# Optimization experiments

Measured on AMD Instinct MI355X. Metric: run time of the kernel, lower is better.

Reference implementation:

```python
import jax, jax.numpy as jnp
import numpy as np

D = 1024          # feature dim (x_dim)
C = 32            # n classes (way)
SHOTS = 32
N_SUP = C * SHOTS
Q = 1024
REG = 0.5         # reg_param


def setup_inputs() -> dict:
    key = jax.random.key(0)
    ks = jax.random.split(key, 5)
    support_x = jax.random.normal(ks[0], (N_SUP, D), dtype=jnp.float32)
    query_x = jax.random.normal(ks[1], (Q, D), dtype=jnp.float32)
    labels_idx = (jnp.arange(N_SUP, dtype=jnp.int32) % C)  # every class present, equal shots
    m = jax.random.normal(ks[2], (1, D), dtype=jnp.float32) * 0.01
    kappa = jnp.float32(0.1)
    nu = jnp.float32(D)
    triu_diag = jnp.ones((D,), dtype=jnp.float32)
    triu_lower = jnp.eye(D, dtype=jnp.float32) + 0.01 * jax.random.normal(ks[3], (D, D), dtype=jnp.float32)
    return {"support_x": support_x, "query_x": query_x, "labels_idx": labels_idx,
            "m": m, "kappa": kappa, "nu": nu,
            "triu_diag": triu_diag, "triu_lower": triu_lower}


def _metaqda_fb(support_x, query_x, labels_idx, m, kappa, nu, triu_diag, triu_lower):
    onehot = jax.nn.one_hot(labels_idx, C, dtype=support_x.dtype)      # [N, C]
    Nj = jnp.sum(onehot, axis=0)                                       # [C]
    kappa_ = jnp.abs(kappa) + 1e-6
    nu_ = jnp.maximum(nu, jnp.float32(D - 1 + 1e-6))

    # Cholesky-factor prior scatter matrix: L @ L^T
    lower_mask = jnp.tril(jnp.ones((D, D), dtype=support_x.dtype), k=-1)
    L = jnp.diag(jnp.abs(triu_diag)) + triu_lower * lower_mask
    prior_S = L @ L.T                                                  # [D, D]

    # per-class sums (replaces python loop of rank-1 outer products with GEMMs)
    sum_x = onehot.T @ support_x                                       # [C, D]
    mean_x = sum_x / Nj[:, None]
    # sum_n x x^T per class: contract through [N,C,D] intermediate
    SXX = jnp.einsum('nc,nd,ne->cde', onehot, support_x, support_x)    # [C, D, D]

    kN = kappa_ + Nj                                                   # [C]
    mu = (kappa_ / kN)[:, None] * m + (Nj / kN)[:, None] * mean_x      # [C, D]

    mm = m.T @ m                                                       # [D, D]  (self_outer of [1,D])
    mumu = jnp.einsum('cd,ce->cde', mu, mu)                            # [C, D, D]
    S = prior_S[None] + SXX + kappa_ * mm[None] - kN[:, None, None] * mumu

    scale = (kN + 1.0) / ((nu_ + Nj - D + 1.0) * kN)                   # [C]
    sigma = S * scale[:, None, None]                                   # [C, D, D]

    sigma_inv = (1.0 - REG) * jnp.linalg.inv(sigma) + REG * jnp.eye(D, dtype=sigma.dtype)

    common = nu_ + Nj + 1.0 - D                                        # [C]
    _, logdet = jnp.linalg.slogdet(sigma)
    bias = (jax.lax.lgamma(0.5 * (common + D)) - jax.lax.lgamma(0.5 * common)
            - 0.5 * D * jnp.log(common) - 0.5 * logdet)                # [C]

    diff = query_x[:, None, :] - mu[None, :, :]                        # [Q, C, D]
    dist = jnp.einsum('qcd,cde,qce->qc', diff, sigma_inv, diff)        # [Q, C]
    preds = bias[None, :] - 0.5 * (common + D)[None, :] * jnp.log1p(dist / common[None, :])
    return preds


def reference(support_x, query_x, labels_idx, m, kappa, nu, triu_diag, triu_lower):
    return _metaqda_fb(support_x, query_x, labels_idx, m, kappa, nu, triu_diag, triu_lower)
```

## Files before the change

### kernel.cpp

```cpp
#include <hip/hip_runtime.h>
#include <math.h>

#define Dk 1024
#define Ck 32
#define Nk 1024
#define Qk 1024
#define REGP 0.5f
#define NB 64
#define NROWSV (Qk + Nk + Ck + 1)

#define CO_KAPPA 0
#define CO_NU    1
#define CO_NJ    2
#define CO_KN    34
#define CO_SCALE 66
#define CO_COMMON 98
#define CO_COEF  130
#define CO_BIASA 162
#define CO_BIASF 200

#define O_P    0u
#define O_W    2162688u
#define O_T    3211264u
#define O_MU   3473408u
#define O_QM   3506176u
#define O_MB   3538944u
#define O_MI   3578112u
#define O_QNY  3617280u
#define O_QNO  3618304u
#define O_MUN  3619328u
#define O_GMM  3619360u
#define O_EX   3619392u
#define O_CONS 3619408u
#define O_CIDX 3619664u
#define O_YH   3652432u
#define O_YM   4733776u
#define O_YL   5815120u
#define O_WH   6896464u
#define O_WM   7420752u
#define O_WL   7945040u
#define O_OH   8469328u
#define O_OM   9550672u
#define O_OL   10632016u

#define WS_DECL \
    float* P     = Wbuf + O_P;    (void)P; \
    float* W     = Wbuf + O_W;    (void)W; \
    float* Tb    = Wbuf + O_T;    (void)Tb; \
    float* QM    = Wbuf + O_QM;   (void)QM; \
    float* Mbuf  = Wbuf + O_MB;   (void)Mbuf; \
    float* Minv  = Wbuf + O_MI;   (void)Minv; \
    float* qny   = Wbuf + O_QNY;  (void)qny; \
    float* qno   = Wbuf + O_QNO;  (void)qno; \
    float* mun2o = Wbuf + O_MUN;  (void)mun2o; \
    float* gmm   = Wbuf + O_GMM;  (void)gmm; \
    float* extraf= Wbuf + O_EX;   (void)extraf; \
    float* cons  = Wbuf + O_CONS; (void)cons; \
    int*   cidx  = (int*)(Wbuf + O_CIDX); (void)cidx; \
    ushort* sYh = (ushort*)(Wbuf + O_YH); (void)sYh; \
    ushort* sYm = (ushort*)(Wbuf + O_YM); (void)sYm; \
    ushort* sYl = (ushort*)(Wbuf + O_YL); (void)sYl; \
    ushort* sWh = (ushort*)(Wbuf + O_WH); (void)sWh; \
    ushort* sWm = (ushort*)(Wbuf + O_WM); (void)sWm; \
    ushort* sWl = (ushort*)(Wbuf + O_WL); (void)sWl; \
    ushort* sOh = (ushort*)(Wbuf + O_OH); (void)sOh; \
    ushort* sOm = (ushort*)(Wbuf + O_OM); (void)sOm; \
    ushort* sOl = (ushort*)(Wbuf + O_OL); (void)sOl;

typedef __attribute__((ext_vector_type(8))) __bf16 bf16x8;
typedef __attribute__((ext_vector_type(4))) float f32x4;

#define MFMA(a, b, c) __builtin_amdgcn_mfma_f32_16x16x32_bf16(a, b, c, 0, 0, 0)

__device__ __forceinline__ ushort f2bf(float x) {
    unsigned u = __float_as_uint(x);
    return (ushort)((u + 0x7FFFu + ((u >> 16) & 1u)) >> 16);
}
__device__ __forceinline__ float bf2f(ushort h) {
    return __uint_as_float(((unsigned)h) << 16);
}
__device__ __forceinline__ void split1(float x, ushort& h, ushort& m, ushort& l) {
    h = f2bf(x);
    float r1 = x - bf2f(h);
    m = f2bf(r1);
    l = f2bf(r1 - bf2f(m));
}
__device__ __forceinline__ void split_store4(ushort* ph, ushort* pm, ushort* pl,
                                             size_t o, float4 v) {
    float vv[4] = {v.x, v.y, v.z, v.w};
    ushort4 H, M, L;
    ushort* Hp = (ushort*)&H; ushort* Mp = (ushort*)&M; ushort* Lp = (ushort*)&L;
#pragma unroll
    for (int c = 0; c < 4; ++c) split1(vv[c], Hp[c], Mp[c], Lp[c]);
    *(ushort4*)(ph + o) = H;
    *(ushort4*)(pm + o) = M;
    *(ushort4*)(pl + o) = L;
}

__device__ __forceinline__ float wave_red(float s) {
#pragma unroll
    for (int o = 32; o > 0; o >>= 1) s += __shfl_down(s, o, 64);
    return s;
}

#define LDSB3(c, r, k8) ((c) * 5120 + (r) * 40 + (k8))
#define LDS_HW3 15360

__device__ __forceinline__ void b_fetch3(bf16x8* rb,
                                         const ushort* Bh, const ushort* Bm, const ushort* Bl,
                                         int bRow0, int kcol, int t) {
#pragma unroll
    for (int u = 0; u < 6; ++u) {
        int comp = u >> 1;
        int idx = ((u & 1) << 8) + t;
        int row = idx >> 2, kg = idx & 3;
        const ushort* Bs = (comp == 0) ? Bh : ((comp == 1) ? Bm : Bl);
        rb[u] = *(const bf16x8*)(Bs + (size_t)(bRow0 + row) * 1024 + kcol + kg * 8);
    }
}
__device__ __forceinline__ void b_store3(ushort* lds, const bf16x8* rb, int t) {
#pragma unroll
    for (int u = 0; u < 6; ++u) {
        int comp = u >> 1;
        int idx = ((u & 1) << 8) + t;
        int row = idx >> 2, kg = idx & 3;
        *(bf16x8*)(lds + LDSB3(comp, row, kg * 8)) = rb[u];
    }
}
__device__ __forceinline__ void a_fetch3(bf16x8 af[4][3],
                                         const ushort* Ah, const ushort* Am, const ushort* Al,
                                         int arowT, int aRowMax, int kcol, int lk) {
    bf16x8 z = {};
#pragma unroll
    for (int rf = 0; rf < 4; ++rf) {
        int gr = arowT + rf * 16;
        bool ok = gr < aRowMax;
#pragma unroll
        for (int c = 0; c < 3; ++c) {
            const ushort* As = (c == 0) ? Ah : ((c == 1) ? Am : Al);
            af[rf][c] = ok ? *(const bf16x8*)(As + (size_t)gr * 1024 + kcol + lk * 8) : z;
        }
    }
}

__device__ __forceinline__ void tile_compute3(const ushort* lds, f32x4 acc[4][4],
                                              bf16x8 af[4][3], int bcol0, int lr, int lk) {
#pragma unroll
    for (int cf = 0; cf < 4; ++cf) {
        int brow = bcol0 + cf * 16 + lr;
        bf16x8 bh = *(const bf16x8*)(lds + LDSB3(0, brow, lk * 8));
        bf16x8 bm = *(const bf16x8*)(lds + LDSB3(1, brow, lk * 8));
        bf16x8 bl = *(const bf16x8*)(lds + LDSB3(2, brow, lk * 8));
#pragma unroll
        for (int rf = 0; rf < 4; ++rf) {
            f32x4 a = acc[rf][cf];
            a = MFMA(af[rf][0], bh, a);
            a = MFMA(af[rf][0], bm, a);
            a = MFMA(af[rf][1], bh, a);
            a = MFMA(af[rf][0], bl, a);
            a = MFMA(af[rf][2], bh, a);
            a = MFMA(af[rf][1], bm, a);
            acc[rf][cf] = a;
        }
    }
}

__device__ __forceinline__ void tile_gemm3(
    ushort* lds, f32x4 acc[4][4],
    const ushort* Ah, const ushort* Am, const ushort* Al, int aRow0, int aRowMax,
    const ushort* Bh, const ushort* Bm, const ushort* Bl, int bRow0,
    int kbase, int ksteps, int t)
{
    const int w = t >> 6, lr = t & 15, lk = (t >> 4) & 3;
    const int arowT = aRow0 + (w >> 1) * 64 + lr;
    const int bcol0 = (w & 1) * 64;
    bf16x8 rb[6], afc[4][3], afn[4][3];
    b_fetch3(rb, Bh, Bm, Bl, bRow0, kbase * 32, t);
    a_fetch3(afc, Ah, Am, Al, arowT, aRowMax, kbase * 32, lk);
    b_store3(lds, rb, t);
    __syncthreads();
    for (int kt = 0; kt < ksteps; ++kt) {
        if (kt + 1 < ksteps) {
            b_fetch3(rb, Bh, Bm, Bl, bRow0, (kbase + kt + 1) * 32, t);
            a_fetch3(afn, Ah, Am, Al, arowT, aRowMax, (kbase + kt + 1) * 32, lk);
        }
        tile_compute3(lds, acc, afc, bcol0, lr, lk);
        __syncthreads();
        if (kt + 1 < ksteps) {
            b_store3(lds, rb, t);
#pragma unroll
            for (int rf = 0; rf < 4; ++rf)
#pragma unroll
                for (int c = 0; c < 3; ++c) afc[rf][c] = afn[rf][c];
        }
        __syncthreads();
    }
}

__device__ __forceinline__ void fetch4(float4* reg, const float* src, int ld,
                                       int rowbase, int rowmax, int colbase, int t) {
#pragma unroll
    for (int u = 0; u < 4; ++u) {
        int slot = t + u * 256;
        int r = slot >> 4, c4 = slot & 15;
        int gr = rowbase + r;
        reg[u] = (gr < rowmax) ? *(const float4*)(src + (size_t)gr * ld + colbase + c4 * 4)
                               : make_float4(0.f, 0.f, 0.f, 0.f);
    }
}
__device__ __forceinline__ void stT(float* dst, const float4* reg, int t) {
#pragma unroll
    for (int u = 0; u < 4; ++u) {
        int slot = t + u * 256;
        int r = slot >> 4, c4 = slot & 15;
        dst[(c4 * 4 + 0) * 68 + r] = reg[u].x;
        dst[(c4 * 4 + 1) * 68 + r] = reg[u].y;
        dst[(c4 * 4 + 2) * 68 + r] = reg[u].z;
        dst[(c4 * 4 + 3) * 68 + r] = reg[u].w;
    }
}
__device__ __forceinline__ void stN(float* dst, const float4* reg, int t) {
#pragma unroll
    for (int u = 0; u < 4; ++u) {
        int slot = t + u * 256;
        int r = slot >> 4, c4 = slot & 15;
        *(float4*)(dst + r * 68 + c4 * 4) = reg[u];
    }
}
__device__ __forceinline__ void gemm16(const float* At, const float* Bt,
                                       float acc[4][4], int tx, int ty) {
#pragma unroll 4
    for (int kk = 0; kk < NB; ++kk) {
        float4 a = *(const float4*)(At + kk * 68 + ty * 4);
        float4 b = *(const float4*)(Bt + kk * 68 + tx * 4);
        float av[4] = {a.x, a.y, a.z, a.w};
        float bv[4] = {b.x, b.y, b.z, b.w};
#pragma unroll
        for (int r = 0; r < 4; ++r)
#pragma unroll
            for (int s = 0; s < 4; ++s) acc[r][s] += av[r] * bv[s];
    }
}
__device__ __forceinline__ void mm_task(
    const float* aSrc, int aLd, int aRow, int aRowMax, int aCol, int aRowStep, int aColStep,
    const float* bSrc, int bLd, int bRow, int bRowMax, int bCol, int bRowStep, int bColStep,
    bool bTrans, int k0, int k1,
    float acc[4][4], float* smA, float* smB, int t, int tx, int ty)
{
    float4 ra[4], rb[4];
    fetch4(ra, aSrc, aLd, aRow + k0 * aRowStep, aRowMax, aCol + k0 * aColStep, t);
    fetch4(rb, bSrc, bLd, bRow + k0 * bRowStep, bRowMax, bCol + k0 * bColStep, t);
    stT(smA, ra, t);
    if (bTrans) stT(smB, rb, t); else stN(smB, rb, t);
    __syncthreads();
    for (int kt = k0; kt < k1; ++kt) {
        if (kt + 1 < k1) {
            fetch4(ra, aSrc, aLd, aRow + (kt + 1) * aRowStep, aRowMax, aCol + (kt + 1) * aColStep, t);
            fetch4(rb, bSrc, bLd, bRow + (kt + 1) * bRowStep, bRowMax, bCol + (kt + 1) * bColStep, t);
        }
        gemm16(smA, smB, acc, tx, ty);
        __syncthreads();
        if (kt + 1 < k1) {
            stT(smA, ra, t);
            if (bTrans) stT(smB, rb, t); else stN(smB, rb, t);
        }
        __syncthreads();
    }
}

__global__ __launch_bounds__(256) void k_p0(const float* qx, const int* labels,
                                            const float* mvec, const float* kappa,
                                            const float* nu, const float* td,
                                            const float* tl, float* Wbuf) {
    __shared__ __align__(16) float smem[9216];
    float* sX  = smem + 8704;
    WS_DECL
    float* Yo32 = Wbuf;
    const int t = threadIdx.x;
    const int lane = t & 63, wv = t >> 6;
    const int tau = blockIdx.x;

    if (tau == 0) {
        int* scnt = (int*)sX;
        if (t < Ck) scnt[t] = 0;
        __syncthreads();
        for (int n = t; n < Nk; n += 256) {
            int l = labels[n];
            int pos = atomicAdd(&scnt[l], 1);
            cidx[l * Nk + pos] = n;
        }
        __syncthreads();
        if (t < Ck) {
            float kap = fabsf(kappa[0]) + 1e-6f;
            float nu_ = fmaxf(nu[0], (float)(Dk - 1) + 1e-6f);
            float Njf = (float)scnt[t];
            float kN = kap + Njf;
            if (t == 0) { cons[CO_KAPPA] = kap; cons[CO_NU] = nu_; }
            cons[CO_NJ + t] = Njf;
            cons[CO_KN + t] = kN;
            cons[CO_SCALE + t] = (kN + 1.0f) / ((nu_ + Njf - (float)Dk + 1.0f) * kN);
            float common = nu_ + Njf + 1.0f - (float)Dk;
            cons[CO_COMMON + t] = common;
            cons[CO_COEF + t] = 0.5f * (common + (float)Dk);
            cons[CO_BIASA + t] = lgammaf(0.5f * (common + (float)Dk)) - lgammaf(0.5f * common)
                                 - 0.5f * (float)Dk * logf(common);
        }
    } else if (tau == 1) {
        float s = 0.f;
        for (int i = t; i < Dk; i += 256) s += logf(fabsf(td[i]));
        s = wave_red(s);
        if (lane == 0) sX[wv] = s;
        __syncthreads();
        if (t == 0) extraf[0] = 2.f * (sX[0] + sX[1] + sX[2] + sX[3]);
    } else if (tau < 18) {
        int b0 = (tau - 2) * NB;
        for (int idx = t; idx < 64 * 64; idx += 256) {
            int m = idx >> 6, i = idx & 63;
            smem[i * 72 + m] = (m > i) ? tl[(size_t)(b0 + m) * Dk + b0 + i] : 0.f;
        }
        if (t < 64) smem[4608 + t] = 1.f / fabsf(td[b0 + t]);
        __syncthreads();
        if (t < 64) {
            const int j = t;
            float r[64];
#pragma unroll
            for (int m = 0; m < 64; ++m) r[m] = (m == j) ? 1.f : 0.f;
#pragma unroll
            for (int i = 0; i < 64; ++i) {
                float x = r[i] * smem[4608 + i];
                r[i] = x;
#pragma unroll
                for (int g = (i >> 2); g < 16; ++g) {
                    float4 lt = *(const float4*)&smem[i * 72 + g * 4];
                    r[g * 4 + 0] -= lt.x * x;
                    r[g * 4 + 1] -= lt.y * x;
                    r[g * 4 + 2] -= lt.z * x;
                    r[g * 4 + 3] -= lt.w * x;
                }
            }
#pragma unroll
            for (int i = 0; i < 64; ++i)
                W[(size_t)(b0 + i) * Dk + b0 + j] = r[i];
        }
    } else if (tau < 21) {
        int base = (tau - 18) * 13056;
        for (int i = t; i < 13056 && base + i < 39168; i += 256) Mbuf[base + i] = 0.f;
    } else if (tau == 21) {
        if (t < 32) { mun2o[t] = 0.f; gmm[t] = 0.f; }
        for (int i = t; i < 8192; i += 256)
            ((float4*)QM)[i] = make_float4(0, 0, 0, 0);
    } else if (tau < 86) {
        int rbase = (tau - 22) * 16;
        for (int j = wv; j < 16; j += 4) {
            const float* row = qx + (size_t)(rbase + j) * Dk;
            float s = 0.f;
            for (int d = lane; d < Dk; d += 64) { float v = row[d]; s += v * v; }
            s = wave_red(s);
            if (lane == 0) qno[rbase + j] = s;
        }
    } else if (tau < 150) {
        int rbase = (tau - 86) * 16;
        for (int j = 0; j < 16; ++j) {
            int r = rbase + j;
            float4 v = ((const float4*)(qx + (size_t)r * Dk))[t];
            split_store4(sYh, sYm, sYl, (size_t)r * 1024 + (size_t)t * 4, v);
        }
    } else if (tau == 150) {
        float4 v = ((const float4*)mvec)[t];
        split_store4(sYh, sYm, sYl, (size_t)2080 * 1024 + (size_t)t * 4, v);
    } else {
        int rbase = (tau - 151) * 16;
        for (int j = 0; j < 16; ++j)
            ((float4*)(Yo32 + (size_t)(rbase + j) * 1024))[t] = make_float4(0, 0, 0, 0);
    }
}

__global__ __launch_bounds__(256) void k_p1(const float* sx, const float* mvec,
                                            const float* tl, float* Wbuf) {
    __shared__ __align__(16) float smem[8704];
    WS_DECL
    const int t = threadIdx.x;
    const int lane = t & 63, wv = t >> 6;
    const int tau = blockIdx.x;
    if (tau < 128) {
        float* sX = smem;
        int c = tau >> 2;
        int d = ((tau & 3) << 8) + t;
        int Nj = (int)cons[CO_NJ + c];
        float kap = cons[CO_KAPPA], kN = cons[CO_KN + c];
        float acc = 0.f;
        for (int s = 0; s < Nj; ++s) acc += sx[(size_t)cidx[c * Nk + s] * Dk + d];
        float muv = (kap * mvec[d] + acc) / kN;
        size_t o = (size_t)(2048 + c) * 1024 + d;
        ushort h, m_, l_;
        split1(muv, h, m_, l_);
        sYh[o] = h; sYm[o] = m_; sYl[o] = l_;
        float s2 = wave_red(muv * muv);
        if (lane == 0) sX[wv] = s2;
        __syncthreads();
        if (t == 0) atomicAdd(&mun2o[c], sX[0] + sX[1] + sX[2] + sX[3]);
    } else if (tau < 192) {
        int rbase = (tau - 128) * 16;
        for (int j = 0; j < 16; ++j) {
            int n = rbase + j;
            int srcrow = cidx[(n >> 5) * Nk + (n & 31)];
            float4 v = ((const float4*)(sx + (size_t)srcrow * Dk))[t];
            split_store4(sYh, sYm, sYl, (size_t)(1024 + n) * 1024 + (size_t)t * 4, v);
        }
    } else {
        float* smA = smem;
        float* smB = smem + 4352;
        const int tx = t & 15, ty = t >> 4;
        const int BIG = 1 << 30;
        int pb = (tau - 192) * 128;
        float acc[4][4] = {};
        mm_task(tl, Dk, pb + 64, BIG, pb, 0, NB,
                W, Dk, pb, BIG, pb, NB, 0, false, 0, 1,
                acc, smA, smB, t, tx, ty);
        {
            float4 ra[4];
            fetch4(ra, W, Dk, pb + 64, BIG, pb + 64, t);
#pragma unroll
            for (int r = 0; r < 4; ++r)
#pragma unroll
                for (int s = 0; s < 4; ++s)
                    smB[(ty * 4 + r) * 68 + tx * 4 + s] = acc[r][s];
            stT(smA, ra, t);
        }
        __syncthreads();
        float acc2[4][4] = {};
        gemm16(smA, smB, acc2, tx, ty);
        __syncthreads();
#pragma unroll
        for (int r = 0; r < 4; ++r)
#pragma unroll
            for (int s = 0; s < 4; ++s)
                W[(size_t)(pb + 64 + ty * 4 + r) * Dk + pb + tx * 4 + s] = -acc2[r][s];
    }
}

__global__ __launch_bounds__(256) void k_tr_a(const float* tl, float* Wbuf, int h, int ht) {
    __shared__ __align__(16) float smem[8704];
    float* smA = smem;
    float* smB = smem + 4352;
    WS_DECL
    const int t = threadIdx.x;
    const int tx = t & 15, ty = t >> 4;
    const int BIG = 1 << 30;
    int tau = blockIdx.x;
    int p = tau / (ht * ht), rr = tau % (ht * ht);
    int i = rr / ht, j = rr % ht;
    int pb = p * 2 * h;
    float acc[4][4] = {};
    mm_task(tl, Dk, pb + h + i * NB, BIG, pb, 0, NB,
            W, Dk, pb, BIG, pb + j * NB, NB, 0, false, 0, ht,
            acc, smA, smB, t, tx, ty);
    float* Tp = Tb + (size_t)p * h * h;
#pragma unroll
    for (int r = 0; r < 4; ++r)
#pragma unroll
        for (int s = 0; s < 4; ++s)
            Tp[(size_t)(i * NB + ty * 4 + r) * h + j * NB + tx * 4 + s] = acc[r][s];
}

__global__ __launch_bounds__(256) void k_tr_b(float* Wbuf, int h, int ht) {
    __shared__ __align__(16) float smem[8704];
    float* smA = smem;
    float* smB = smem + 4352;
    WS_DECL
    const int t = threadIdx.x;
    const int tx = t & 15, ty = t >> 4;
    const int BIG = 1 << 30;
    int tau = blockIdx.x;
    int p = tau / (ht * ht), rr = tau % (ht * ht);
    int i = rr / ht, j = rr % ht;
    int pb = p * 2 * h;
    const float* Tp = Tb + (size_t)p * h * h;
    float acc[4][4] = {};
    mm_task(W, Dk, pb + h + i * NB, BIG, pb + h, 0, NB,
            Tp, h, 0, BIG, j * NB, NB, 0, false, 0, ht,
            acc, smA, smB, t, tx, ty);
#pragma unroll
    for (int r = 0; r < 4; ++r)
#pragma unroll
        for (int s = 0; s < 4; ++s)
            W[(size_t)(pb + h + i * NB + ty * 4 + r) * Dk + pb + j * NB + tx * 4 + s] = -acc[r][s];
}

__global__ __launch_bounds__(256) void k_cvtw(float* Wbuf) {
    WS_DECL
    const int t = threadIdx.x;
#pragma unroll
    for (int u = 0; u < 4; ++u) {
        unsigned g = blockIdx.x * 1024u + u * 256u + t;
        int row = g >> 8, col4 = (g & 255) * 4;
        float4 v = ((const float4*)W)[g];
        if (col4 + 0 > row) v.x = 0.f;
        if (col4 + 1 > row) v.y = 0.f;
        if (col4 + 2 > row) v.z = 0.f;
        if (col4 + 3 > row) v.w = 0.f;
        split_store4(sWh, sWm, sWl, (size_t)g * 4, v);
    }
}

__global__ __launch_bounds__(256) void k_yg(float* Wbuf) {
    __shared__ __align__(16) ushort lds[LDS_HW3];
    WS_DECL
    float* Yo32 = Wbuf;
    const int t = threadIdx.x;
    int b = blockIdx.x;
    int xcd = b & 7, pos = b >> 3;
    int e = (xcd < 4) ? xcd * 43 + pos : 172 + (xcd - 4) * 42 + pos;
    int q = e / 17, rt = e % 17;
    int jt2, kc;
    if (q < 4)       { jt2 = 7; kc = q; }
    else if (q < 8)  { jt2 = 6; kc = q - 4; }
    else if (q < 11) { jt2 = 5; kc = q - 8; }
    else if (q < 14) { jt2 = 4; kc = q - 11; }
    else if (q < 16) { jt2 = 3; kc = q - 14; }
    else if (q < 18) { jt2 = 2; kc = q - 16; }
    else if (q == 18){ jt2 = 1; kc = 0; }
    else             { jt2 = 0; kc = 0; }
    int ksteps = min(8, 4 * (jt2 + 1) - kc * 8);
    f32x4 acc[4][4] = {};
    tile_gemm3(lds, acc, sYh, sYm, sYl, rt * 128, 2081,
               sWh, sWm, sWl, jt2 * 128, kc * 8, ksteps, t);
    const int w = t >> 6, lr = t & 15, lk = (t >> 4) & 3;
#pragma unroll
    for (int rf = 0; rf < 4; ++rf)
#pragma unroll
        for (int cf = 0; cf < 4; ++cf)
#pragma unroll
            for (int r = 0; r < 4; ++r) {
                int grow = rt * 128 + (w >> 1) * 64 + rf * 16 + lk * 4 + r;
                if (grow < NROWSV)
                    atomicAdd(&Yo32[(size_t)grow * 1024 + jt2 * 128 + (w & 1) * 64 + cf * 16 + lr],
                              acc[rf][cf][r]);
            }
}

__global__ __launch_bounds__(256) void k_cvto(float* Wbuf) {
    WS_DECL
    float* Yo32 = Wbuf;
    const int t = threadIdx.x;
    int rbase = blockIdx.x * 4;
#pragma unroll
    for (int j = 0; j < 4; ++j) {
        int r = rbase + j;
        float4 v = ((const float4*)(Yo32 + (size_t)r * 1024))[t];
        split_store4(sOh, sOm, sOl, (size_t)r * 1024 + (size_t)t * 4, v);
    }
    if (rbase < 1088) {
#pragma unroll
        for (int j = 0; j < 4; ++j)
            ((float4*)(Yo32 + (size_t)(rbase + j) * 1024))[t] = make_float4(0, 0, 0, 0);
    }
}

__global__ __launch_bounds__(256) void k_p4m(float* Wbuf) {
    __shared__ __align__(16) ushort lds[LDS_HW3];
    WS_DECL
    const int t = threadIdx.x;
    int b = blockIdx.x;
    int e = (b & 7) * 40 + (b >> 3);
    const int w = t >> 6, lr = t & 15, lk = (t >> 4) & 3;
    f32x4 acc[4][4] = {};
    if (e < 288) {
        int qt2 = e / 36, rem = e % 36;
        int mt = rem >> 2, kc = rem & 3;
        tile_gemm3(lds, acc, sOh, sOm, sOl, 1024 + mt * 128, 2081,
                   sOh, sOm, sOl, qt2 * 128, kc * 8, 8, t);
#pragma unroll
        for (int rf = 0; rf < 4; ++rf)
#pragma unroll
            for (int cf = 0; cf < 4; ++cf)
#pragma unroll
                for (int r = 0; r < 4; ++r) {
                    int n = mt * 128 + (w >> 1) * 64 + rf * 16 + lk * 4 + r;
                    if (n < Nk + Ck + 1)
                        atomicAdd(&P[(size_t)n * 1024 + qt2 * 128 + (w & 1) * 64 + cf * 16 + lr],
                                  acc[rf][cf][r]);
                }
    } else {
        int f = e - 288;
        int qt2 = f >> 2, kc = f & 3;
        tile_gemm3(lds, acc, sYh, sYm, sYl, 2048, 2080,
                   sYh, sYm, sYl, qt2 * 128, kc * 8, 8, t);
#pragma unroll
        for (int rf = 0; rf < 4; ++rf)
#pragma unroll
            for (int cf = 0; cf < 4; ++cf)
#pragma unroll
                for (int r = 0; r < 4; ++r) {
                    int rq = (w >> 1) * 64 + rf * 16 + lk * 4 + r;
                    if (rq < 32)
                        atomicAdd(&QM[(size_t)rq * 1024 + qt2 * 128 + (w & 1) * 64 + cf * 16 + lr],
                                  acc[rf][cf][r]);
                }
    }
}

__global__ __launch_bounds__(256) void k_gram(float* Wbuf) {
    __shared__ __align__(16) float smA[34 * 68];
    WS_DECL
    const int t = threadIdx.x;
    const int lane = t & 63, wv = t >> 6;
    const int tau = blockIdx.x;
    if (tau < 128) {
        int c = tau >> 2, kc = tau & 3;
        float accg[5];
        int iu[5], ju[5];
#pragma unroll
        for (int u = 0; u < 5; ++u) {
            int e = t + u * 256;
            iu[u] = e / 34; ju[u] = e - iu[u] * 34;
            accg[u] = 0.f;
        }
        for (int kt = kc * 4; kt < kc * 4 + 4; ++kt) {
            for (int e2 = t; e2 < 34 * NB; e2 += 256) {
                int i = e2 >> 6, k = e2 & 63;
                int yr = (i < 32) ? (Qk + c * 32 + i) : ((i == 32) ? (Qk + Nk + c) : (Qk + Nk + Ck));
                size_t o = (size_t)yr * 1024 + kt * NB + k;
                smA[i * 68 + k] = bf2f(sOh[o]) + bf2f(sOm[o]) + bf2f(sOl[o]);
            }
            __syncthreads();
#pragma unroll
            for (int u = 0; u < 5; ++u) {
                int e = t + u * 256;
                if (e < 1156) {
                    float s = 0.f;
                    for (int k = 0; k < NB; ++k) s += smA[iu[u] * 68 + k] * smA[ju[u] * 68 + k];
                    accg[u] += s;
                }
            }
            __syncthreads();
        }
#pragma unroll
        for (int u = 0; u < 5; ++u) {
            int e = t + u * 256;
            if (e < 1156)
                atomicAdd(&Mbuf[c * 1224 + iu[u] * 36 + ju[u]], accg[u]);
        }
    } else {
        int rbase = (tau - 128) * 16;
        for (int j = wv; j < 16; j += 4) {
            size_t ro = (size_t)(rbase + j) * 1024;
            float s = 0.f;
            for (int d = lane; d < Dk; d += 64) {
                size_t o = ro + d;
                float v = bf2f(sOh[o]) + bf2f(sOm[o]) + bf2f(sOl[o]);
                s += v * v;
            }
            s = wave_red(s);
            if (lane == 0) qny[rbase + j] = s;
        }
    }
}

__global__ __launch_bounds__(64) void k_p5(float* Wbuf) {
    __shared__ __align__(16) float A[34 * 36];
    WS_DECL
    const int t = threadIdx.x;
    const int c = blockIdx.x;
    float kN = cons[CO_KN + c], kap = cons[CO_KAPPA];
    for (int e = t; e < 34 * 34; e += 64) {
        int i = e / 34, j = e - i * 34;
        A[i * 36 + j] = Mbuf[c * 1224 + i * 36 + j];
    }
    __syncthreads();
    if (t == 0) {
        gmm[c] = A[32 * 36 + 32];
        A[32 * 36 + 32] += -1.f / kN;
        A[33 * 36 + 33] += 1.f / kap;
    }
    if (t < 32) A[t * 36 + t] += 1.f;
    __syncthreads();
    float ldacc = 0.f;
    for (int j = 0; j < 34; ++j) {
        float piv = A[j * 36 + j];
        float pinv = 1.f / piv;
        if (t == 0) ldacc += logf(fabsf(piv));
        if (t < 34 && t != j) A[j * 36 + t] *= pinv;
        __syncthreads();
        if (t < 34) {
            if (t != j) {
                float f = A[t * 36 + j];
                float4* rowT = (float4*)(A + t * 36);
                const float4* rowJ = (const float4*)(A + j * 36);
#pragma unroll
                for (int k4 = 0; k4 < 8; ++k4) {
                    float4 rv = rowT[k4], pv = rowJ[k4];
                    rv.x -= f * pv.x; rv.y -= f * pv.y;
                    rv.z -= f * pv.z; rv.w -= f * pv.w;
                    rowT[k4] = rv;
                }
                A[t * 36 + 32] -= f * A[j * 36 + 32];
                A[t * 36 + 33] -= f * A[j * 36 + 33];
                A[t * 36 + j] = -f * pinv;
            } else {
                A[j * 36 + j] = pinv;
            }
        }
        __syncthreads();
    }
    for (int e = t; e < 34 * 34; e += 64) {
        int i = e / 34, j = e - i * 34;
        Minv[c * 1224 + i * 36 + j] = A[i * 36 + j];
    }
    if (t == 0) {
        float scale = cons[CO_SCALE + c];
        float logdet = (float)Dk * logf(scale) + extraf[0] + logf(kN) + logf(kap) + ldacc;
        cons[CO_BIASF + c] = cons[CO_BIASA + c] - 0.5f * logdet;
    }
}

__global__ __launch_bounds__(256) void k_p6(float* Wbuf, float* out) {
    __shared__ __align__(16) float smem[3904];
    float* Mi  = smem;
    float* wL  = smem + 1200;
    float* gsm = smem + 3520;
    float* red = smem + 3520 + 128;
    WS_DECL
    const int t = threadIdx.x;
    const int tau = blockIdx.x;
    int qt = tau >> 5, c = tau & 31;
    for (int e = t; e < 34 * 34; e += 256) {
        int i = e / 34, j = e - i * 34;
        Mi[i * 35 + j] = Minv[c * 1224 + i * 36 + j];
    }
    if (t < 34)
        gsm[t] = (t < 32) ? Mbuf[c * 1224 + t * 36 + 32]
                          : ((t == 32) ? gmm[c] : Mbuf[c * 1224 + 33 * 36 + 32]);
    __syncthreads();
    for (int e = t; e < 34 * NB; e += 256) {
        int i = e >> 6, qq = e & 63;
        int prow = (i < 32) ? (c * 32 + i) : ((i == 32) ? (Nk + c) : (Nk + Ck));
        wL[i * 68 + qq] = P[(size_t)prow * Qk + qt * NB + qq] - gsm[i];
    }
    __syncthreads();
    {
        int q = t & 63, part = t >> 6;
        int start = (part < 2) ? part * 9 : 18 + (part - 2) * 8;
        int cnt = (part < 2) ? 9 : 8;
        float partial = 0.f;
        for (int i = start; i < start + cnt; ++i) {
            float v = 0.f;
            for (int j = 0; j < 34; ++j) v += Mi[i * 35 + j] * wL[j * 68 + q];
            partial += v * wL[i * 68 + q];
        }
        red[part * 64 + q] = partial;
    }
    __syncthreads();
    if (t < 64) {
        int q = t;
        float quad = red[q] + red[64 + q] + red[128 + q] + red[192 + q];
        int qg = qt * NB + q;
        float w32 = wL[32 * 68 + q];
        float ydist2 = qny[qg] - 2.f * w32 - gmm[c];
        float dd = qno[qg] + mun2o[c] - 2.f * QM[(size_t)c * Qk + qg];
        float scale = cons[CO_SCALE + c], common = cons[CO_COMMON + c];
        float dist = (1.f - REGP) / scale * (ydist2 - quad) + REGP * dd;
        out[(size_t)qg * Ck + c] = cons[CO_BIASF + c] - cons[CO_COEF + c] * log1pf(dist / common);
    }
}

extern "C" void kernel_launch(void* const* d_in, const int* in_sizes, int n_in,
                              void* d_out, int out_size, void* d_ws, size_t ws_size,
                              hipStream_t stream) {
    const float* sx = (const float*)d_in[0];
    const float* qx = (const float*)d_in[1];
    const int* labels = (const int*)d_in[2];
    const float* mvec = (const float*)d_in[3];
    const float* kappa = (const float*)d_in[4];
    const float* nu = (const float*)d_in[5];
    const float* td = (const float*)d_in[6];
    const float* tl = (const float*)d_in[7];
    float* W = (float*)d_ws;
    float* out = (float*)d_out;

    hipLaunchKernelGGL(k_p0, dim3(283), dim3(256), 0, stream,
                       qx, labels, mvec, kappa, nu, td, tl, W);
    hipLaunchKernelGGL(k_p1, dim3(200), dim3(256), 0, stream, sx, mvec, tl, W);
    for (int l = 2; l <= 4; ++l) {
        int h = 32 << l, ht = h >> 6, pairs = 16 >> l;
        int nt = pairs * ht * ht;
        hipLaunchKernelGGL(k_tr_a, dim3(nt), dim3(256), 0, stream, tl, W, h, ht);
        hipLaunchKernelGGL(k_tr_b, dim3(nt), dim3(256), 0, stream, W, h, ht);
    }
    hipLaunchKernelGGL(k_cvtw, dim3(256), dim3(256), 0, stream, W);
    hipLaunchKernelGGL(k_yg, dim3(340), dim3(256), 0, stream, W);
    hipLaunchKernelGGL(k_cvto, dim3(528), dim3(256), 0, stream, W);
    hipLaunchKernelGGL(k_p4m, dim3(320), dim3(256), 0, stream, W);
    hipLaunchKernelGGL(k_gram, dim3(192), dim3(256), 0, stream, W);
    hipLaunchKernelGGL(k_p5, dim3(32), dim3(64), 0, stream, W);
    hipLaunchKernelGGL(k_p6, dim3(512), dim3(256), 0, stream, W, out);
}
```

Before: 354.9 us.

## Double-buffer LDS in split-bf16 GEMM and fuse query norms into conversion

The tiled three-way split-bf16 GEMM now ping-pongs between two LDS buffers, which removes one of the two barriers per k-step so stores of the next tile can overlap compute on the current one. The squared norms of the first 1024 output rows are now computed in k_cvto from the fp32 values it already loads, instead of in a separate block range of k_gram that re-read and recombined the three bf16 parts. This drops 64 blocks from k_gram. LDS use per GEMM block doubles, which may reduce occupancy. The qny zeroing was added as well, though the norms are now written directly rather than accumulated.

```diff
diff --git a/kernel.cpp b/kernel.cpp
--- a/kernel.cpp
+++ b/kernel.cpp
@@ -104,7 +104,8 @@
 }
 
 #define LDSB3(c, r, k8) ((c) * 5120 + (r) * 40 + (k8))
-#define LDS_HW3 15360
+#define LDS_BUF 15360
+#define LDS_HW3 30720
 
 __device__ __forceinline__ void b_fetch3(bf16x8* rb,
                                          const ushort* Bh, const ushort* Bm, const ushort* Bl,
@@ -118,13 +119,13 @@
         rb[u] = *(const bf16x8*)(Bs + (size_t)(bRow0 + row) * 1024 + kcol + kg * 8);
     }
 }
-__device__ __forceinline__ void b_store3(ushort* lds, const bf16x8* rb, int t) {
+__device__ __forceinline__ void b_store3(ushort* ldsb, const bf16x8* rb, int t) {
 #pragma unroll
     for (int u = 0; u < 6; ++u) {
         int comp = u >> 1;
         int idx = ((u & 1) << 8) + t;
         int row = idx >> 2, kg = idx & 3;
-        *(bf16x8*)(lds + LDSB3(comp, row, kg * 8)) = rb[u];
+        *(bf16x8*)(ldsb + LDSB3(comp, row, kg * 8)) = rb[u];
     }
 }
 __device__ __forceinline__ void a_fetch3(bf16x8 af[4][3],
@@ -143,14 +144,14 @@
     }
 }
 
-__device__ __forceinline__ void tile_compute3(const ushort* lds, f32x4 acc[4][4],
+__device__ __forceinline__ void tile_compute3(const ushort* ldsb, f32x4 acc[4][4],
                                               bf16x8 af[4][3], int bcol0, int lr, int lk) {
 #pragma unroll
     for (int cf = 0; cf < 4; ++cf) {
         int brow = bcol0 + cf * 16 + lr;
-        bf16x8 bh = *(const bf16x8*)(lds + LDSB3(0, brow, lk * 8));
-        bf16x8 bm = *(const bf16x8*)(lds + LDSB3(1, brow, lk * 8));
-        bf16x8 bl = *(const bf16x8*)(lds + LDSB3(2, brow, lk * 8));
+        bf16x8 bh = *(const bf16x8*)(ldsb + LDSB3(0, brow, lk * 8));
+        bf16x8 bm = *(const bf16x8*)(ldsb + LDSB3(1, brow, lk * 8));
+        bf16x8 bl = *(const bf16x8*)(ldsb + LDSB3(2, brow, lk * 8));
 #pragma unroll
         for (int rf = 0; rf < 4; ++rf) {
             f32x4 a = acc[rf][cf];
@@ -180,14 +181,15 @@
     b_store3(lds, rb, t);
     __syncthreads();
     for (int kt = 0; kt < ksteps; ++kt) {
+        ushort* cur = lds + (kt & 1) * LDS_BUF;
+        ushort* nxt = lds + ((kt + 1) & 1) * LDS_BUF;
         if (kt + 1 < ksteps) {
             b_fetch3(rb, Bh, Bm, Bl, bRow0, (kbase + kt + 1) * 32, t);
             a_fetch3(afn, Ah, Am, Al, arowT, aRowMax, (kbase + kt + 1) * 32, lk);
         }
-        tile_compute3(lds, acc, afc, bcol0, lr, lk);
-        __syncthreads();
+        tile_compute3(cur, acc, afc, bcol0, lr, lk);
         if (kt + 1 < ksteps) {
-            b_store3(lds, rb, t);
+            b_store3(nxt, rb, t);
 #pragma unroll
             for (int rf = 0; rf < 4; ++rf)
 #pragma unroll
@@ -349,6 +351,7 @@
         if (t < 32) { mun2o[t] = 0.f; gmm[t] = 0.f; }
         for (int i = t; i < 8192; i += 256)
             ((float4*)QM)[i] = make_float4(0, 0, 0, 0);
+        if (t < 256) ((float4*)qny)[t] = make_float4(0, 0, 0, 0);
     } else if (tau < 86) {
         int rbase = (tau - 22) * 16;
         for (int j = wv; j < 16; j += 4) {
@@ -540,15 +543,31 @@
 }
 
 __global__ __launch_bounds__(256) void k_cvto(float* Wbuf) {
+    __shared__ float sred[16];
     WS_DECL
     float* Yo32 = Wbuf;
     const int t = threadIdx.x;
+    const int lane = t & 63, wv = t >> 6;
     int rbase = blockIdx.x * 4;
+    float4 vv[4];
 #pragma unroll
     for (int j = 0; j < 4; ++j) {
         int r = rbase + j;
         float4 v = ((const float4*)(Yo32 + (size_t)r * 1024))[t];
+        vv[j] = v;
         split_store4(sOh, sOm, sOl, (size_t)r * 1024 + (size_t)t * 4, v);
+    }
+    if (rbase < 1024) {
+#pragma unroll
+        for (int j = 0; j < 4; ++j) {
+            float4 v = vv[j];
+            float s = v.x * v.x + v.y * v.y + v.z * v.z + v.w * v.w;
+            s = wave_red(s);
+            if (lane == 0) sred[wv * 4 + j] = s;
+        }
+        __syncthreads();
+        if (t < 4)
+            qny[rbase + t] = sred[t] + sred[4 + t] + sred[8 + t] + sred[12 + t];
     }
     if (rbase < 1088) {
 #pragma unroll
@@ -604,56 +623,40 @@
     __shared__ __align__(16) float smA[34 * 68];
     WS_DECL
     const int t = threadIdx.x;
-    const int lane = t & 63, wv = t >> 6;
     const int tau = blockIdx.x;
-    if (tau < 128) {
-        int c = tau >> 2, kc = tau & 3;
-        float accg[5];
-        int iu[5], ju[5];
+    int c = tau >> 2, kc = tau & 3;
+    float accg[5];
+    int iu[5], ju[5];
+#pragma unroll
+    for (int u = 0; u < 5; ++u) {
+        int e = t + u * 256;
+        iu[u] = e / 34; ju[u] = e - iu[u] * 34;
+        accg[u] = 0.f;
+    }
+    for (int kt = kc * 4; kt < kc * 4 + 4; ++kt) {
+        for (int e2 = t; e2 < 34 * NB; e2 += 256) {
+            int i = e2 >> 6, k = e2 & 63;
+            int yr = (i < 32) ? (Qk + c * 32 + i) : ((i == 32) ? (Qk + Nk + c) : (Qk + Nk + Ck));
+            size_t o = (size_t)yr * 1024 + kt * NB + k;
+            smA[i * 68 + k] = bf2f(sOh[o]) + bf2f(sOm[o]) + bf2f(sOl[o]);
+        }
+        __syncthreads();
 #pragma unroll
         for (int u = 0; u < 5; ++u) {
             int e = t + u * 256;
-            iu[u] = e / 34; ju[u] = e - iu[u] * 34;
-            accg[u] = 0.f;
-        }
-        for (int kt = kc * 4; kt < kc * 4 + 4; ++kt) {
-            for (int e2 = t; e2 < 34 * NB; e2 += 256) {
-                int i = e2 >> 6, k = e2 & 63;
-                int yr = (i < 32) ? (Qk + c * 32 + i) : ((i == 32) ? (Qk + Nk + c) : (Qk + Nk + Ck));
-                size_t o = (size_t)yr * 1024 + kt * NB + k;
-                smA[i * 68 + k] = bf2f(sOh[o]) + bf2f(sOm[o]) + bf2f(sOl[o]);
+            if (e < 1156) {
+                float s = 0.f;
+                for (int k = 0; k < NB; ++k) s += smA[iu[u] * 68 + k] * smA[ju[u] * 68 + k];
+                accg[u] += s;
             }
-            __syncthreads();
-#pragma unroll
-            for (int u = 0; u < 5; ++u) {
-                int e = t + u * 256;
-                if (e < 1156) {
-                    float s = 0.f;
-                    for (int k = 0; k < NB; ++k) s += smA[iu[u] * 68 + k] * smA[ju[u] * 68 + k];
-                    accg[u] += s;
-                }
-            }
-            __syncthreads();
-        }
-#pragma unroll
-        for (int u = 0; u < 5; ++u) {
-            int e = t + u * 256;
-            if (e < 1156)
-                atomicAdd(&Mbuf[c * 1224 + iu[u] * 36 + ju[u]], accg[u]);
-        }
-    } else {
-        int rbase = (tau - 128) * 16;
-        for (int j = wv; j < 16; j += 4) {
-            size_t ro = (size_t)(rbase + j) * 1024;
-            float s = 0.f;
-            for (int d = lane; d < Dk; d += 64) {
-                size_t o = ro + d;
-                float v = bf2f(sOh[o]) + bf2f(sOm[o]) + bf2f(sOl[o]);
-                s += v * v;
-            }
-            s = wave_red(s);
-            if (lane == 0) qny[rbase + j] = s;
-        }
+        }
+        __syncthreads();
+    }
+#pragma unroll
+    for (int u = 0; u < 5; ++u) {
+        int e = t + u * 256;
+        if (e < 1156)
+            atomicAdd(&Mbuf[c * 1224 + iu[u] * 36 + ju[u]], accg[u]);
     }
 }
 
@@ -791,7 +794,7 @@
     hipLaunchKernelGGL(k_yg, dim3(340), dim3(256), 0, stream, W);
     hipLaunchKernelGGL(k_cvto, dim3(528), dim3(256), 0, stream, W);
     hipLaunchKernelGGL(k_p4m, dim3(320), dim3(256), 0, stream, W);
-    hipLaunchKernelGGL(k_gram, dim3(192), dim3(256), 0, stream, W);
+    hipLaunchKernelGGL(k_gram, dim3(128), dim3(256), 0, stream, W);
     hipLaunchKernelGGL(k_p5, dim3(32), dim3(64), 0, stream, W);
     hipLaunchKernelGGL(k_p6, dim3(512), dim3(256), 0, stream, W, out);
 }
```

After: 398.5 us. +12.3%, slower.
